# Optimization experiments

Measured on AMD Instinct MI355X. Metric: run time of the kernel, lower is better.

## Reference

```python
import jax, jax.numpy as jnp
import numpy as np

KH = KW = 3
STRIDE = 1
PAD = 1
DIL = 1


def _bilinear_sample(img, py, px):
    Hin, Win = img.shape[-2], img.shape[-1]
    y0 = jnp.floor(py)
    x0 = jnp.floor(px)
    y0i = y0.astype(jnp.int32)
    x0i = x0.astype(jnp.int32)
    wy = py - y0
    wx = px - x0

    def get(yi, xi):
        valid = (yi >= 0) & (yi < Hin) & (xi >= 0) & (xi < Win)
        yc = jnp.clip(yi, 0, Hin - 1)
        xc = jnp.clip(xi, 0, Win - 1)
        v = img[:, yc, xc]  # [C, K, H, W]
        return v * valid[None].astype(img.dtype)

    v00 = get(y0i, x0i)
    v01 = get(y0i, x0i + 1)
    v10 = get(y0i + 1, x0i)
    v11 = get(y0i + 1, x0i + 1)
    return (v00 * (1 - wy) * (1 - wx) + v01 * (1 - wy) * wx
            + v10 * wy * (1 - wx) + v11 * wy * wx)  # [C, K, H, W]


def _deform_conv(input, offset, mask, weight, bias):
    B, C, H, W = input.shape
    outH = (H + 2 * PAD - DIL * (KH - 1) - 1) // STRIDE + 1
    outW = (W + 2 * PAD - DIL * (KW - 1) - 1) // STRIDE + 1
    K = KH * KW
    # NOTE: DepthOffset in the original source overwrites its computed
    # depth-guided offsets with zeros and detaches them, so the effective
    # sampling offset is just `offset` (standard modulated deform conv, DCNv2).
    off = offset.reshape(B, K, 2, outH, outW)
    off_y = off[:, :, 0]  # [B, K, outH, outW]
    off_x = off[:, :, 1]
    ky = (jnp.arange(K) // KW) * DIL  # kernel-tap row offsets
    kx = (jnp.arange(K) % KW) * DIL
    ys = jnp.arange(outH) * STRIDE - PAD
    xs = jnp.arange(outW) * STRIDE - PAD
    base_y = (ky[:, None, None] + ys[None, :, None]).astype(input.dtype)  # [K, outH, 1]
    base_x = (kx[:, None, None] + xs[None, None, :]).astype(input.dtype)  # [K, 1, outW]
    py = base_y[None] + off_y  # [B, K, outH, outW]
    px = base_x[None] + off_x
    cols = jax.vmap(_bilinear_sample)(input, py, px)  # [B, C, K, outH, outW]
    cols = cols * mask[:, None]  # modulate by mask [B, 1, K, outH, outW]
    out = jnp.einsum('bckhw,ock->bohw', cols, weight.reshape(weight.shape[0], C, K))
    return out + bias[None, :, None, None]


def setup_inputs() -> dict:
    key = jax.random.key(0)
    ks = jax.random.split(key, 6)
    B, C, H, W = 4, 64, 128, 128
    O = 64
    fan_in = C * KH * KW
    bound = 1.0 / np.sqrt(fan_in)
    return {
        'input': jax.random.normal(ks[0], (B, C, H, W), dtype=jnp.float32),
        'depth': jax.random.uniform(ks[1], (B, 1, H, W), dtype=jnp.float32),
        'offset': jax.random.normal(ks[2], (B, 18, H, W), dtype=jnp.float32),
        'mask': jax.random.uniform(ks[3], (B, 9, H, W), dtype=jnp.float32),
        'weight': jax.random.uniform(ks[4], (O, C, KH, KW), dtype=jnp.float32,
                                     minval=-bound, maxval=bound),
        'bias': jax.random.uniform(ks[5], (O,), dtype=jnp.float32,
                                   minval=-bound, maxval=bound),
    }


def reference(input, depth, offset, mask, weight, bias):
    # depth-guided offsets are computed then zeroed+detached in the original
    # module, so depth does not influence the output.
    return _deform_conv(input, offset, mask, weight, bias)
```

## Files before the change

kernel.cpp:

```cpp
#include <hip/hip_runtime.h>


typedef __attribute__((ext_vector_type(8))) short bf16x8;
typedef __attribute__((ext_vector_type(4))) float f32x4;
typedef __attribute__((ext_vector_type(4))) unsigned int u32x4;

#define HH 128
#define WW 128
#define CC 64
#define OO 64
#define HW (128 * 128)

__device__ __forceinline__ unsigned f32_to_bf16_rne(float f) {
    unsigned u = __float_as_uint(f);
    return (u + 0x7FFFu + ((u >> 16) & 1u)) >> 16;
}

__global__ __launch_bounds__(256)
void prep_fused12(const float* __restrict__ input,
                  unsigned short* __restrict__ nhwc,
                  const float* __restrict__ weight,
                  unsigned short* __restrict__ wT2)
{
    __shared__ unsigned tile[64][33];
    const int tid = threadIdx.x;
    const int blk = blockIdx.x;

    if (blk >= 2048) {
        const int d  = (blk - 2048) * 256 + tid;
        const int o  = d & 63;
        const int k8 = d >> 6;
        const int kt = k8 >> 3;
        const int c8 = k8 & 7;
        u32x4 pk;
        #pragma unroll
        for (int jj = 0; jj < 4; ++jj) {
            unsigned lo = f32_to_bf16_rne(weight[o * 576 + (c8 * 8 + 2 * jj)     * 9 + kt]);
            unsigned hi = f32_to_bf16_rne(weight[o * 576 + (c8 * 8 + 2 * jj + 1) * 9 + kt]);
            pk[jj] = lo | (hi << 16);
        }
        *(u32x4*)(wT2 + (size_t)d * 8) = pk;
        return;
    }

    const int b  = blk >> 9;
    const int y  = (blk >> 2) & 127;
    const int xbase = (blk & 3) * 32;
    #pragma unroll
    for (int it = 0; it < 8; ++it) {
        int flat = it * 256 + tid;
        int c = flat >> 5, x = flat & 31;
        float v = input[((b * 64 + c) * 128 + y) * 128 + xbase + x];
        tile[c][x] = f32_to_bf16_rne(v);
    }
    __syncthreads();
    {
        int x = tid >> 3, cg = tid & 7;
        unsigned r0 = tile[cg * 8 + 0][x], r1 = tile[cg * 8 + 1][x];
        unsigned r2 = tile[cg * 8 + 2][x], r3 = tile[cg * 8 + 3][x];
        unsigned r4 = tile[cg * 8 + 4][x], r5 = tile[cg * 8 + 5][x];
        unsigned r6 = tile[cg * 8 + 6][x], r7 = tile[cg * 8 + 7][x];
        u32x4 pk;
        pk[0] = r0 | (r1 << 16); pk[1] = r2 | (r3 << 16);
        pk[2] = r4 | (r5 << 16); pk[3] = r6 | (r7 << 16);
        *(u32x4*)(nhwc + ((size_t)((b * 128 + y) * 128 + xbase + x)) * 64 + cg * 8) = pk;
    }
}

__global__ __launch_bounds__(1024, 4)
void ddc_win12(const unsigned short* __restrict__ nhwc,
               const unsigned short* __restrict__ wT2,
               const float* __restrict__ offset,
               const float* __restrict__ mask,
               const float* __restrict__ bias,
               float* __restrict__ out)
{
    __shared__ u32x4 win[9216];

    const int blk0 = blockIdx.x;
    const int blk  = (blk0 & 7) * 32 + (blk0 >> 3);
    const int b    = blk >> 6;
    const int h0   = (blk & 63) * 2;
    const int ys   = h0 - 3;
    const int tid  = threadIdx.x;
    const int wave = tid >> 6;
    const int lane = tid & 63;
    const int l15  = lane & 15;
    const int kq   = lane >> 4;
    const int h    = h0 + (wave >> 3);
    const int wpix = (wave & 7) * 16 + l15;

    f32x4 acc[4];
    #pragma unroll
    for (int mt = 0; mt < 4; ++mt) acc[mt] = (f32x4){0.f, 0.f, 0.f, 0.f};

    const unsigned short* nb = nhwc + (size_t)b * HW * CC;
    const u32x4* wsrc = (const u32x4*)wT2;

    float oyv[9], oxv[9], mv[9];
    #pragma unroll
    for (int kt = 0; kt < 9; ++kt) {
        oyv[kt] = offset[((b * 18 + 2 * kt)     * 128 + h) * 128 + wpix];
        oxv[kt] = offset[((b * 18 + 2 * kt + 1) * 128 + h) * 128 + wpix];
        mv[kt]  = mask  [((b * 9  + kt)         * 128 + h) * 128 + wpix];
    }

    #pragma unroll
    for (int slot = 0; slot < 9; ++slot) {
        const int y = ys + slot;
        if (y >= 0 && y < HH) {
            const int q  = tid;
            const int x  = q >> 3;
            const int c8 = q & 7;
            win[slot * 1024 + q] =
                *(const u32x4*)(nb + ((size_t)(y * WW + x)) * CC + ((c8 ^ (x & 7)) << 3));
        }
    }
    __syncthreads();

    auto do_tap = [&](int kt, float oy, float ox, float m) {
        const float py = (float)(h - 1 + kt / 3) + oy;
        const float px = (float)(wpix - 1 + kt % 3) + ox;
        const float y0f = floorf(py), x0f = floorf(px);
        const int y0 = (int)y0f, x0 = (int)x0f;
        const float wy = py - y0f, wx = px - x0f;
        const int y1 = y0 + 1, x1 = x0 + 1;
        const bool vy0 = (y0 >= 0) & (y0 < HH);
        const bool vy1 = (y1 >= 0) & (y1 < HH);
        const bool vx0 = (x0 >= 0) & (x0 < WW);
        const bool vx1 = (x1 >= 0) & (x1 < WW);
        const int y0c = min(max(y0, 0), HH - 1), y1c = min(max(y1, 0), HH - 1);
        const int x0c = min(max(x0, 0), WW - 1), x1c = min(max(x1, 0), WW - 1);
        const float wy1 = 1.f - wy, wx1 = 1.f - wx;
        const float c00 = (vy0 && vx0) ? wy1 * wx1 * m : 0.f;
        const float c01 = (vy0 && vx1) ? wy1 * wx  * m : 0.f;
        const float c10 = (vy1 && vx0) ? wy  * wx1 * m : 0.f;
        const float c11 = (vy1 && vx1) ? wy  * wx  * m : 0.f;

        const int s0 = y0c - ys, s1 = y1c - ys;
        const bool in0 = ((unsigned)s0 < 9u);
        const bool in1 = ((unsigned)s1 < 9u);
        const int r0 = (in0 ? s0 : 0) * 1024;
        const int r1 = (in1 ? s1 : 0) * 1024;
        const int bx0 = x0c * 8, sx0 = x0c & 7;
        const int bx1 = x1c * 8, sx1 = x1c & 7;

        #pragma unroll
        for (int ks = 0; ks < 2; ++ks) {
            const int ch = ks * 4 + kq;

            u32x4 w00 = win[r0 + bx0 + (ch ^ sx0)];
            u32x4 w01 = win[r0 + bx1 + (ch ^ sx1)];
            u32x4 w10 = win[r1 + bx0 + (ch ^ sx0)];
            u32x4 w11 = win[r1 + bx1 + (ch ^ sx1)];
            if (!in0) {
                w00 = *(const u32x4*)(nb + ((size_t)y0c * WW + x0c) * CC + ch * 8);
                w01 = *(const u32x4*)(nb + ((size_t)y0c * WW + x1c) * CC + ch * 8);
            }
            if (!in1) {
                w10 = *(const u32x4*)(nb + ((size_t)y1c * WW + x0c) * CC + ch * 8);
                w11 = *(const u32x4*)(nb + ((size_t)y1c * WW + x1c) * CC + ch * 8);
            }

            u32x4 pk;
            #pragma unroll
            for (int j = 0; j < 4; ++j) {
                const float a0 = __uint_as_float(w00[j] << 16);
                const float a1 = __uint_as_float(w00[j] & 0xFFFF0000u);
                const float b0 = __uint_as_float(w01[j] << 16);
                const float b1 = __uint_as_float(w01[j] & 0xFFFF0000u);
                const float d0 = __uint_as_float(w10[j] << 16);
                const float d1 = __uint_as_float(w10[j] & 0xFFFF0000u);
                const float e0 = __uint_as_float(w11[j] << 16);
                const float e1 = __uint_as_float(w11[j] & 0xFFFF0000u);
                const float s0f = c00 * a0 + c01 * b0 + c10 * d0 + c11 * e0;
                const float s1f = c00 * a1 + c01 * b1 + c10 * d1 + c11 * e1;
                pk[j] = f32_to_bf16_rne(s0f) | (f32_to_bf16_rne(s1f) << 16);
            }
            const bf16x8 bfrag = __builtin_bit_cast(bf16x8, pk);

            #pragma unroll
            for (int mt = 0; mt < 4; ++mt) {
                const bf16x8 afrag = __builtin_bit_cast(bf16x8,
                    wsrc[(kt * 8 + ks * 4 + kq) * 64 + mt * 16 + l15]);
                acc[mt] = __builtin_amdgcn_mfma_f32_16x16x32_bf16(afrag, bfrag, acc[mt], 0, 0, 0);
            }
        }
    };

    #pragma unroll
    for (int kt = 0; kt < 9; ++kt) {
        do_tap(kt, oyv[kt], oxv[kt], mv[kt]);
    }

    #pragma unroll
    for (int mt = 0; mt < 4; ++mt) {
        const f32x4 bv = *(const f32x4*)(bias + mt * 16 + kq * 4);
        #pragma unroll
        for (int r = 0; r < 4; ++r) {
            const int o = mt * 16 + kq * 4 + r;
            out[((b * 64 + o) * 128 + h) * 128 + wpix] = acc[mt][r] + bv[r];
        }
    }
}

extern "C" void kernel_launch(void* const* d_in, const int* in_sizes, int n_in,
                              void* d_out, int out_size, void* d_ws, size_t ws_size,
                              hipStream_t stream)
{
    const float* input  = (const float*)d_in[0];
    const float* offset = (const float*)d_in[2];
    const float* mask   = (const float*)d_in[3];
    const float* weight = (const float*)d_in[4];
    const float* bias   = (const float*)d_in[5];
    float* out = (float*)d_out;

    unsigned short* nhwc = (unsigned short*)d_ws;
    unsigned short* wT2  = nhwc + (size_t)4 * HW * CC;

    prep_fused12<<<dim3(2066), dim3(256), 0, stream>>>(input, nhwc, weight, wT2);
    ddc_win12<<<dim3(256), dim3(1024), 0, stream>>>(nhwc, wT2, offset, mask, bias, out);
}
```

Measured before the change: 105.4 us.

## Stage offsets/mask in LDS, shrink row window, use packed FMA and bf16 convert

The main kernel now loads each block's offset and mask planes cooperatively into shared memory instead of holding 27 per-thread values in registers. The input row window shrinks from 9 to 8 rows; samples outside it fall back to global loads. Bilinear blending uses 2-wide float vectors, and bf16 packing uses the hardware v_cvt_pk_bf16_f32 instruction. The prep kernel reads the input with float4 loads, and the launch-bounds occupancy hint is dropped. The aim is less register pressure and fewer ALU instructions, at the cost of more LDS traffic and possibly more global fallback loads.

```diff
diff --git a/kernel.cpp b/kernel.cpp
--- a/kernel.cpp
+++ b/kernel.cpp
@@ -3,6 +3,7 @@
 
 typedef __attribute__((ext_vector_type(8))) short bf16x8;
 typedef __attribute__((ext_vector_type(4))) float f32x4;
+typedef __attribute__((ext_vector_type(2))) float f32x2;
 typedef __attribute__((ext_vector_type(4))) unsigned int u32x4;
 
 #define HH 128
@@ -17,7 +18,7 @@
 }
 
 __global__ __launch_bounds__(256)
-void prep_fused12(const float* __restrict__ input,
+void prep_fused15(const float* __restrict__ input,
                   unsigned short* __restrict__ nhwc,
                   const float* __restrict__ weight,
                   unsigned short* __restrict__ wT2)
@@ -47,11 +48,14 @@
     const int y  = (blk >> 2) & 127;
     const int xbase = (blk & 3) * 32;
     #pragma unroll
-    for (int it = 0; it < 8; ++it) {
+    for (int it = 0; it < 2; ++it) {
         int flat = it * 256 + tid;
-        int c = flat >> 5, x = flat & 31;
-        float v = input[((b * 64 + c) * 128 + y) * 128 + xbase + x];
-        tile[c][x] = f32_to_bf16_rne(v);
+        int c = flat >> 3, x4 = flat & 7;
+        const f32x4 v = *(const f32x4*)(input + ((b * 64 + c) * 128 + y) * 128 + xbase + x4 * 4);
+        tile[c][x4 * 4 + 0] = f32_to_bf16_rne(v[0]);
+        tile[c][x4 * 4 + 1] = f32_to_bf16_rne(v[1]);
+        tile[c][x4 * 4 + 2] = f32_to_bf16_rne(v[2]);
+        tile[c][x4 * 4 + 3] = f32_to_bf16_rne(v[3]);
     }
     __syncthreads();
     {
@@ -67,15 +71,16 @@
     }
 }
 
-__global__ __launch_bounds__(1024, 4)
-void ddc_win12(const unsigned short* __restrict__ nhwc,
-               const unsigned short* __restrict__ wT2,
-               const float* __restrict__ offset,
-               const float* __restrict__ mask,
-               const float* __restrict__ bias,
-               float* __restrict__ out)
+__global__ __launch_bounds__(1024)
+void ddc_slim15(const unsigned short* __restrict__ nhwc,
+                const unsigned short* __restrict__ wT2,
+                const float* __restrict__ offset,
+                const float* __restrict__ mask,
+                const float* __restrict__ bias,
+                float* __restrict__ out)
 {
-    __shared__ u32x4 win[9216];
+    __shared__ u32x4 win[8192];
+    __shared__ float sten[6912];
 
     const int blk0 = blockIdx.x;
     const int blk  = (blk0 & 7) * 32 + (blk0 >> 3);
@@ -87,7 +92,8 @@
     const int lane = tid & 63;
     const int l15  = lane & 15;
     const int kq   = lane >> 4;
-    const int h    = h0 + (wave >> 3);
+    const int hr   = wave >> 3;
+    const int h    = h0 + hr;
     const int wpix = (wave & 7) * 16 + l15;
 
     f32x4 acc[4];
@@ -97,16 +103,21 @@
     const unsigned short* nb = nhwc + (size_t)b * HW * CC;
     const u32x4* wsrc = (const u32x4*)wT2;
 
-    float oyv[9], oxv[9], mv[9];
-    #pragma unroll
-    for (int kt = 0; kt < 9; ++kt) {
-        oyv[kt] = offset[((b * 18 + 2 * kt)     * 128 + h) * 128 + wpix];
-        oxv[kt] = offset[((b * 18 + 2 * kt + 1) * 128 + h) * 128 + wpix];
-        mv[kt]  = mask  [((b * 9  + kt)         * 128 + h) * 128 + wpix];
-    }
-
-    #pragma unroll
-    for (int slot = 0; slot < 9; ++slot) {
+    #pragma unroll
+    for (int it = 0; it < 7; ++it) {
+        const int f = it * 1024 + tid;
+        if (f < 6912) {
+            const int plane = f >> 8;
+            const int fr    = (f >> 7) & 1;
+            const int x     = f & 127;
+            sten[f] = (plane < 18)
+                ? offset[((b * 18 + plane)      * 128 + (h0 + fr)) * 128 + x]
+                : mask  [((b * 9 + (plane - 18))* 128 + (h0 + fr)) * 128 + x];
+        }
+    }
+
+    #pragma unroll
+    for (int slot = 0; slot < 8; ++slot) {
         const int y = ys + slot;
         if (y >= 0 && y < HH) {
             const int q  = tid;
@@ -118,7 +129,12 @@
     }
     __syncthreads();
 
-    auto do_tap = [&](int kt, float oy, float ox, float m) {
+    #pragma unroll
+    for (int kt = 0; kt < 9; ++kt) {
+        const float oy = sten[(2 * kt)     * 256 + hr * 128 + wpix];
+        const float ox = sten[(2 * kt + 1) * 256 + hr * 128 + wpix];
+        const float m  = sten[(18 + kt)    * 256 + hr * 128 + wpix];
+
         const float py = (float)(h - 1 + kt / 3) + oy;
         const float px = (float)(wpix - 1 + kt % 3) + ox;
         const float y0f = floorf(py), x0f = floorf(px);
@@ -138,12 +154,15 @@
         const float c11 = (vy1 && vx1) ? wy  * wx  * m : 0.f;
 
         const int s0 = y0c - ys, s1 = y1c - ys;
-        const bool in0 = ((unsigned)s0 < 9u);
-        const bool in1 = ((unsigned)s1 < 9u);
+        const bool in0 = ((unsigned)s0 < 8u);
+        const bool in1 = ((unsigned)s1 < 8u);
         const int r0 = (in0 ? s0 : 0) * 1024;
         const int r1 = (in1 ? s1 : 0) * 1024;
         const int bx0 = x0c * 8, sx0 = x0c & 7;
         const int bx1 = x1c * 8, sx1 = x1c & 7;
+
+        const f32x2 vc00 = (f32x2){c00, c00}, vc01 = (f32x2){c01, c01};
+        const f32x2 vc10 = (f32x2){c10, c10}, vc11 = (f32x2){c11, c11};
 
         #pragma unroll
         for (int ks = 0; ks < 2; ++ks) {
@@ -165,32 +184,31 @@
             u32x4 pk;
             #pragma unroll
             for (int j = 0; j < 4; ++j) {
-                const float a0 = __uint_as_float(w00[j] << 16);
-                const float a1 = __uint_as_float(w00[j] & 0xFFFF0000u);
-                const float b0 = __uint_as_float(w01[j] << 16);
-                const float b1 = __uint_as_float(w01[j] & 0xFFFF0000u);
-                const float d0 = __uint_as_float(w10[j] << 16);
-                const float d1 = __uint_as_float(w10[j] & 0xFFFF0000u);
-                const float e0 = __uint_as_float(w11[j] << 16);
-                const float e1 = __uint_as_float(w11[j] & 0xFFFF0000u);
-                const float s0f = c00 * a0 + c01 * b0 + c10 * d0 + c11 * e0;
-                const float s1f = c00 * a1 + c01 * b1 + c10 * d1 + c11 * e1;
-                pk[j] = f32_to_bf16_rne(s0f) | (f32_to_bf16_rne(s1f) << 16);
+                const f32x2 A = (f32x2){__uint_as_float(w00[j] << 16),
+                                        __uint_as_float(w00[j] & 0xFFFF0000u)};
+                const f32x2 B = (f32x2){__uint_as_float(w01[j] << 16),
+                                        __uint_as_float(w01[j] & 0xFFFF0000u)};
+                const f32x2 D = (f32x2){__uint_as_float(w10[j] << 16),
+                                        __uint_as_float(w10[j] & 0xFFFF0000u)};
+                const f32x2 E = (f32x2){__uint_as_float(w11[j] << 16),
+                                        __uint_as_float(w11[j] & 0xFFFF0000u)};
+                const f32x2 S = vc00 * A + vc01 * B + vc10 * D + vc11 * E;
+                unsigned r;
+                asm("v_cvt_pk_bf16_f32 %0, %1, %2" : "=v"(r) : "v"(S[0]), "v"(S[1]));
+                pk[j] = r;
             }
             const bf16x8 bfrag = __builtin_bit_cast(bf16x8, pk);
 
-            #pragma unroll
-            for (int mt = 0; mt < 4; ++mt) {
-                const bf16x8 afrag = __builtin_bit_cast(bf16x8,
-                    wsrc[(kt * 8 + ks * 4 + kq) * 64 + mt * 16 + l15]);
-                acc[mt] = __builtin_amdgcn_mfma_f32_16x16x32_bf16(afrag, bfrag, acc[mt], 0, 0, 0);
-            }
-        }
-    };
-
-    #pragma unroll
-    for (int kt = 0; kt < 9; ++kt) {
-        do_tap(kt, oyv[kt], oxv[kt], mv[kt]);
+            const u32x4* wp = wsrc + (kt * 8 + ks * 4 + kq) * 64 + l15;
+            acc[0] = __builtin_amdgcn_mfma_f32_16x16x32_bf16(
+                __builtin_bit_cast(bf16x8, wp[0]),  bfrag, acc[0], 0, 0, 0);
+            acc[1] = __builtin_amdgcn_mfma_f32_16x16x32_bf16(
+                __builtin_bit_cast(bf16x8, wp[16]), bfrag, acc[1], 0, 0, 0);
+            acc[2] = __builtin_amdgcn_mfma_f32_16x16x32_bf16(
+                __builtin_bit_cast(bf16x8, wp[32]), bfrag, acc[2], 0, 0, 0);
+            acc[3] = __builtin_amdgcn_mfma_f32_16x16x32_bf16(
+                __builtin_bit_cast(bf16x8, wp[48]), bfrag, acc[3], 0, 0, 0);
+        }
     }
 
     #pragma unroll
@@ -218,6 +236,6 @@
     unsigned short* nhwc = (unsigned short*)d_ws;
     unsigned short* wT2  = nhwc + (size_t)4 * HW * CC;
 
-    prep_fused12<<<dim3(2066), dim3(256), 0, stream>>>(input, nhwc, weight, wT2);
-    ddc_win12<<<dim3(256), dim3(1024), 0, stream>>>(nhwc, wT2, offset, mask, bias, out);
-}
+    prep_fused15<<<dim3(2066), dim3(256), 0, stream>>>(input, nhwc, weight, wT2);
+    ddc_slim15<<<dim3(256), dim3(1024), 0, stream>>>(nhwc, wT2, offset, mask, bias, out);
+}
```

Measured after the change: 104.6 us. Within noise of the previous version (-0.7%).
